# Kernel optimization log

Measured on AMD Instinct MI355X. Metric: run time of the kernel, lower is better.

## Reference

```python
import jax, jax.numpy as jnp
import numpy as np

EMB_W, COMMIT_W, ENT_W = 1.0, 0.25, 0.1  # loss weights from init_kwargs


def setup_inputs() -> dict:
    key = jax.random.key(0)
    k1, k2 = jax.random.split(key)
    B, H, W, D, K = 32, 32, 32, 64, 1024
    inputs = jax.random.normal(k1, (B, H, W, D), dtype=jnp.float32)
    # keras RandomUniform default: U(-0.05, 0.05)
    codebook = jax.random.uniform(k2, (K, D), dtype=jnp.float32, minval=-0.05, maxval=0.05)
    return {"inputs": inputs, "codebook": codebook}


def reference(inputs, codebook):
    # inputs: [B,H,W,D], codebook: [K,D]
    D = inputs.shape[-1]
    x = inputs.reshape(-1, D)  # [N,D]
    dist = (
        jnp.sum(x * x, axis=-1, keepdims=True)
        - 2.0 * (x @ codebook.T)
        + jnp.sum(codebook * codebook, axis=-1)
    )  # [N,K]
    tokens = jnp.argmin(dist, axis=-1)  # [N]
    emb = codebook[tokens].reshape(inputs.shape)  # [B,H,W,D]

    embedding_loss = EMB_W * jnp.mean((jax.lax.stop_gradient(emb) - inputs) ** 2)
    commitment_loss = COMMIT_W * jnp.mean((emb - jax.lax.stop_gradient(inputs)) ** 2)
    # 'entropy' loss as written in call(): mean over codebook of per-code min distance
    entropy_loss = ENT_W * jnp.mean(jnp.min(dist, axis=0))
    loss = embedding_loss + commitment_loss + entropy_loss

    # training=True path: straight-through estimator
    out = inputs + jax.lax.stop_gradient(emb - inputs)
    return out, loss
```

## Files before the change

### kernel.cpp

```cpp
#include <hip/hip_runtime.h>
#include <math.h>

#define NROWS 32768
#define NCODE 1024
#define AMB_CAP 8192
#define GAP_THRESH 1.5e-4f

typedef __attribute__((ext_vector_type(8))) short bf16x8;
typedef __attribute__((ext_vector_type(4))) float f32x4;

__device__ __forceinline__ unsigned short bf16_rne(float f) {
    unsigned u = __float_as_uint(f);
    unsigned r = u + 0x7FFFu + ((u >> 16) & 1u);
    return (unsigned short)(r >> 16);
}

typedef const __attribute__((address_space(1))) unsigned GU;
typedef __attribute__((address_space(3))) unsigned LU;
__device__ __forceinline__ void gl_lds16(const void* g, void* l) {
    __builtin_amdgcn_global_load_lds((GU*)g, (LU*)l, 16, 0, 0);
}
__device__ __forceinline__ void gl_lds4(const void* g, void* l) {
    __builtin_amdgcn_global_load_lds((GU*)g, (LU*)l, 4, 0, 0);
}

__global__ __launch_bounds__(256) void vq_prep(
    const float* __restrict__ cb, float* __restrict__ cn4,
    unsigned* __restrict__ minK, unsigned* __restrict__ counter,
    float* __restrict__ gsumsq, unsigned* __restrict__ ticket,
    unsigned short* __restrict__ wsB)
{
    int c = blockIdx.x * 256 + threadIdx.x;
    if (c == 0) { *counter = 0u; *gsumsq = 0.f; *ticket = 0u; }
    if (c >= NCODE) return;
    float v[64];
    const float4* src = (const float4*)(cb + (size_t)c * 64);
    float s = 0.f;
    #pragma unroll
    for (int i = 0; i < 16; i++) {
        float4 t = src[i];
        v[i*4+0] = t.x; v[i*4+1] = t.y; v[i*4+2] = t.z; v[i*4+3] = t.w;
        s += t.x*t.x + t.y*t.y + t.z*t.z + t.w*t.w;
    }
    cn4[c] = s + 4.0f;
    minK[c] = 0x7F800000u;
    int cc = c >> 6, ct = (c >> 4) & 3, cl = c & 15;
    #pragma unroll
    for (int q = 0; q < 4; q++) {
        int half = q & 1, lo = q >> 1;
        #pragma unroll
        for (int g = 0; g < 4; g++) {
            unsigned short u8[8] __attribute__((aligned(16)));
            #pragma unroll
            for (int j = 0; j < 8; j++) {
                float f = v[half*32 + g*8 + j];
                unsigned short h = bf16_rne(f);
                if (lo) h = bf16_rne(f - __uint_as_float((unsigned)h << 16));
                u8[j] = h;
            }
            size_t off = (size_t)cc * 8192 + ct * 2048 + q * 512 + (g * 16 + cl) * 8;
            *(uint4*)(wsB + off) = *(const uint4*)u8;
        }
    }
}

__global__ __launch_bounds__(256, 4) void vq_main(
    const float* __restrict__ x, const float* __restrict__ cb,
    const unsigned short* __restrict__ wsB, const float* __restrict__ cn4,
    float* __restrict__ out, unsigned* __restrict__ minK,
    unsigned* __restrict__ counter, int* __restrict__ amb,
    float* __restrict__ gsumsq)
{
    __shared__ __align__(16) unsigned char Bb[2][16384];
    __shared__ float cn4L[2][64];
    __shared__ unsigned scrE[1024];
    __shared__ int   tokS[64];
    __shared__ float redS[4];

    const int tid = threadIdx.x;
    const int lane = tid & 63;
    const int wi = tid >> 6;
    const int ln15 = lane & 15;
    const int q = lane >> 4;
    const int row0 = blockIdx.x * 64;
    const int rot = blockIdx.x & 15;

    #pragma unroll
    for (int jj = 0; jj < 4; jj++) scrE[jj*256 + tid] = 0x7F800000u;

    const char* wsBb = (const char*)wsB;
    {
        int wbase = (tid & ~63) * 16;
        #pragma unroll
        for (int i = 0; i < 4; i++)
            gl_lds16(wsBb + rot*16384 + (i*256 + tid)*16, (void*)&Bb[0][i*4096 + wbase]);
        if (wi == 0) gl_lds4(cn4 + rot*64 + lane, (void*)&cn4L[0][0]);
    }

    bf16x8 Ah0, Ah1, Al0, Al1;
    float xnm4[4];
    {
        const float* xr = x + (size_t)(row0 + wi*16 + ln15) * 64 + q * 8;
        float4 f0 = *(const float4*)xr;
        float4 f1 = *(const float4*)(xr + 4);
        float4 f2 = *(const float4*)(xr + 32);
        float4 f3 = *(const float4*)(xr + 36);
        float fa[8] = {f0.x,f0.y,f0.z,f0.w,f1.x,f1.y,f1.z,f1.w};
        float fb[8] = {f2.x,f2.y,f2.z,f2.w,f3.x,f3.y,f3.z,f3.w};
        unsigned short h[8]  __attribute__((aligned(16)));
        unsigned short l[8]  __attribute__((aligned(16)));
        unsigned short h2[8] __attribute__((aligned(16)));
        unsigned short l2[8] __attribute__((aligned(16)));
        float ss = 0.f;
        #pragma unroll
        for (int j = 0; j < 8; j++) {
            ss += fa[j]*fa[j] + fb[j]*fb[j];
            unsigned short hh = bf16_rne(fa[j]);
            h[j] = hh; l[j] = bf16_rne(fa[j] - __uint_as_float((unsigned)hh << 16));
            hh = bf16_rne(fb[j]);
            h2[j] = hh; l2[j] = bf16_rne(fb[j] - __uint_as_float((unsigned)hh << 16));
        }
        Ah0 = *(const bf16x8*)h;  Al0 = *(const bf16x8*)l;
        Ah1 = *(const bf16x8*)h2; Al1 = *(const bf16x8*)l2;
        ss += __shfl_xor(ss, 16);
        ss += __shfl_xor(ss, 32);
        #pragma unroll
        for (int r = 0; r < 4; r++)
            xnm4[r] = __shfl(ss, (q << 2) | r, 64) - 4.0f;
    }

    float d1[4], d2[4];
    int   i1[4];
    #pragma unroll
    for (int r = 0; r < 4; r++) { d1[r] = INFINITY; d2[r] = INFINITY; i1[r] = 0; }

    for (int s = 0; s < 16; s++) {
        __syncthreads();
        const int cb_ = s & 1, nb = (s + 1) & 1;
        const int cphys = (s + rot) & 15;
        if (s < 15) {
            const int cnx = (s + 1 + rot) & 15;
            int wbase = (tid & ~63) * 16;
            #pragma unroll
            for (int i = 0; i < 4; i++)
                gl_lds16(wsBb + cnx*16384 + (i*256 + tid)*16,
                         (void*)&Bb[nb][i*4096 + wbase]);
            if (wi == 0) gl_lds4(cn4 + cnx*64 + lane, (void*)&cn4L[nb][0]);
        }
        const unsigned char* buf = Bb[cb_];
        #pragma unroll
        for (int ct = 0; ct < 4; ct++) {
            bf16x8 Bh0 = *(const bf16x8*)(buf + ct*4096 +    0 + lane*16);
            bf16x8 Bh1 = *(const bf16x8*)(buf + ct*4096 + 1024 + lane*16);
            bf16x8 Bl0 = *(const bf16x8*)(buf + ct*4096 + 2048 + lane*16);
            bf16x8 Bl1 = *(const bf16x8*)(buf + ct*4096 + 3072 + lane*16);
            float cn4v = cn4L[cb_][ct*16 + ln15];
            int kid = cphys*64 + ct*16 + ln15;
            f32x4 acc = {0.f, 0.f, 0.f, 0.f};
            acc = __builtin_amdgcn_mfma_f32_16x16x32_bf16(Ah0, Bh0, acc, 0, 0, 0);
            acc = __builtin_amdgcn_mfma_f32_16x16x32_bf16(Ah1, Bh1, acc, 0, 0, 0);
            acc = __builtin_amdgcn_mfma_f32_16x16x32_bf16(Ah0, Bl0, acc, 0, 0, 0);
            acc = __builtin_amdgcn_mfma_f32_16x16x32_bf16(Ah1, Bl1, acc, 0, 0, 0);
            acc = __builtin_amdgcn_mfma_f32_16x16x32_bf16(Al0, Bh0, acc, 0, 0, 0);
            acc = __builtin_amdgcn_mfma_f32_16x16x32_bf16(Al1, Bh1, acc, 0, 0, 0);
            float cminv = INFINITY;
            #pragma unroll
            for (int r = 0; r < 4; r++) {
                float wv = fmaf(acc[r], -2.0f, cn4v);
                bool lt = wv < d1[r];
                d2[r] = lt ? d1[r] : fminf(d2[r], wv);
                i1[r] = lt ? kid   : i1[r];
                d1[r] = lt ? wv    : d1[r];
                cminv = fminf(cminv, wv + xnm4[r]);
            }
            cminv = fminf(cminv, __shfl_xor(cminv, 16));
            cminv = fminf(cminv, __shfl_xor(cminv, 32));
            if (q == ct) atomicMin(&scrE[kid], __float_as_uint(cminv));
        }
    }
    __syncthreads();

    #pragma unroll
    for (int d = 1; d < 16; d <<= 1) {
        #pragma unroll
        for (int r = 0; r < 4; r++) {
            float od1 = __shfl_xor(d1[r], d);
            int   oi1 = __shfl_xor(i1[r], d);
            float od2 = __shfl_xor(d2[r], d);
            bool take = (od1 < d1[r]) || (od1 == d1[r] && oi1 < i1[r]);
            float loser = take ? d1[r] : od1;
            d2[r] = fminf(fminf(d2[r], od2), loser);
            d1[r] = take ? od1 : d1[r];
            i1[r] = take ? oi1 : i1[r];
        }
    }
    if (ln15 == 0) {
        #pragma unroll
        for (int r = 0; r < 4; r++) {
            tokS[wi*16 + q*4 + r] = i1[r];
            if (d2[r] - d1[r] < GAP_THRESH) {
                unsigned idx = atomicAdd(counter, 1u);
                if (idx < AMB_CAP) {
                    amb[2*idx]   = row0 + wi*16 + q*4 + r;
                    amb[2*idx+1] = i1[r];
                }
            }
        }
    }
    __syncthreads();

    #pragma unroll
    for (int jj = 0; jj < 4; jj++) {
        int c = jj*256 + tid;
        unsigned u = scrE[c];
        if (u < minK[c]) atomicMin(&minK[c], u);
    }

    {
        int grow = tid >> 2, p = tid & 3;
        int tok = tokS[grow];
        const float4* cv = (const float4*)(cb + (size_t)tok*64 + p*16);
        const float4* xv = (const float4*)(x  + (size_t)(row0 + grow)*64 + p*16);
        float4* ov = (float4*)(out + (size_t)(row0 + grow)*64 + p*16);
        float acc2 = 0.f;
        #pragma unroll
        for (int i = 0; i < 4; i++) {
            float4 c = cv[i]; float4 xx = xv[i];
            ov[i] = c;
            float dx = c.x-xx.x, dy = c.y-xx.y, dz = c.z-xx.z, dw = c.w-xx.w;
            acc2 += dx*dx + dy*dy + dz*dz + dw*dw;
        }
        #pragma unroll
        for (int o = 32; o > 0; o >>= 1) acc2 += __shfl_down(acc2, o);
        if ((tid & 63) == 0) redS[tid >> 6] = acc2;
        __syncthreads();
        if (tid == 0) atomicAdd(gsumsq, redS[0] + redS[1] + redS[2] + redS[3]);
    }
}

__global__ __launch_bounds__(256) void vq_tail(
    const float* __restrict__ x, const float* __restrict__ cb,
    float* __restrict__ out, const unsigned* __restrict__ counter,
    const int* __restrict__ amb, float* __restrict__ gsumsq,
    unsigned* __restrict__ ticket, const unsigned* __restrict__ minK,
    float* __restrict__ out_loss)
{
    __shared__ double xs[64];
    __shared__ double bd[256];
    __shared__ int    bi[256];
    __shared__ unsigned lastS;
    __shared__ float redS[4];

    const int tid = threadIdx.x;

    unsigned cnt = *counter; if (cnt > AMB_CAP) cnt = AMB_CAP;
    for (unsigned i = blockIdx.x; i < cnt; i += gridDim.x) {
        int row = amb[2*i], oldk = amb[2*i+1];
        __syncthreads();
        if (tid < 64) xs[tid] = (double)x[(size_t)row*64 + tid];
        __syncthreads();
        double xn = 0.0;
        #pragma unroll 8
        for (int d = 0; d < 64; d++) xn += xs[d]*xs[d];
        double best = INFINITY; int bk = 1 << 30;
        #pragma unroll
        for (int j = 0; j < 4; j++) {
            int k = j*256 + tid;
            const float4* c4 = (const float4*)(cb + (size_t)k*64);
            double dot = 0.0, cn2 = 0.0;
            #pragma unroll
            for (int t = 0; t < 16; t++) {
                float4 cv = c4[t];
                double cx = (double)cv.x, cy = (double)cv.y, cz = (double)cv.z, cw = (double)cv.w;
                dot += xs[t*4+0]*cx + xs[t*4+1]*cy + xs[t*4+2]*cz + xs[t*4+3]*cw;
                cn2 += cx*cx + cy*cy + cz*cz + cw*cw;
            }
            double dist = (xn - 2.0*dot) + cn2;
            if (dist < best || (dist == best && k < bk)) { best = dist; bk = k; }
        }
        bd[tid] = best; bi[tid] = bk;
        __syncthreads();
        for (int s = 128; s > 0; s >>= 1) {
            if (tid < s) {
                double od = bd[tid+s]; int ok = bi[tid+s];
                if (od < bd[tid] || (od == bd[tid] && ok < bi[tid])) { bd[tid] = od; bi[tid] = ok; }
            }
            __syncthreads();
        }
        int bestk = bi[0];
        if (bestk != oldk) {
            double part = 0.0;
            if (tid < 64) {
                float cn = cb[(size_t)bestk*64 + tid];
                float co = cb[(size_t)oldk*64 + tid];
                out[(size_t)row*64 + tid] = cn;
                double dn = (double)cn - xs[tid];
                double dl = (double)co - xs[tid];
                part = dn*dn - dl*dl;
            }
            __syncthreads();
            bd[tid] = part;
            __syncthreads();
            for (int s = 128; s > 0; s >>= 1) {
                if (tid < s) bd[tid] += bd[tid+s];
                __syncthreads();
            }
            if (tid == 0) atomicAdd(gsumsq, (float)bd[0]);
        }
    }

    __syncthreads();
    if (tid == 0) {
        __threadfence();
        lastS = (atomicAdd(ticket, 1u) == (unsigned)(gridDim.x - 1)) ? 1u : 0u;
    }
    __syncthreads();
    if (lastS) {
        __threadfence();
        float s = 0.f;
        #pragma unroll
        for (int jj = 0; jj < 4; jj++)
            s += __uint_as_float(minK[jj*256 + tid]);
        #pragma unroll
        for (int o = 32; o > 0; o >>= 1) s += __shfl_down(s, o);
        if ((tid & 63) == 0) redS[tid >> 6] = s;
        __syncthreads();
        if (tid == 0) {
            float gs = atomicAdd(gsumsq, 0.0f);
            float tot = redS[0] + redS[1] + redS[2] + redS[3];
            out_loss[0] = 1.25f * (gs / 2097152.0f) + 0.1f * (tot / 1024.0f);
        }
    }
}

extern "C" void kernel_launch(void* const* d_in, const int* in_sizes, int n_in,
                              void* d_out, int out_size, void* d_ws, size_t ws_size,
                              hipStream_t stream) {
    const float* x  = (const float*)d_in[0];
    const float* cb = (const float*)d_in[1];
    float* out = (float*)d_out;

    char* ws = (char*)d_ws;
    unsigned*       counter = (unsigned*)ws;
    float*          gsumsq  = (float*)(ws + 4);
    unsigned*       ticket  = (unsigned*)(ws + 8);
    float*          cn4     = (float*)(ws + 1024);
    unsigned*       minK    = (unsigned*)(ws + 8192);
    int*            amb     = (int*)(ws + 16384);
    unsigned short* wsB     = (unsigned short*)(ws + 131072);

    vq_prep<<<4,   256, 0, stream>>>(cb, cn4, minK, counter, gsumsq, ticket, wsB);
    vq_main<<<512, 256, 0, stream>>>(x, cb, wsB, cn4, out, minK, counter, amb, gsumsq);
    vq_tail<<<64,  256, 0, stream>>>(x, cb, out, counter, amb, gsumsq, ticket, minK,
                                     out + 2097152);
}
```

Measured before the change: 136.2 us.

## Split codebook tiles across wave pairs with 512-thread blocks and merge argmins

Doubles the main kernel's block size to 8 waves. Each pair of waves now shares 16 input rows, and each wave of the pair processes half of every 64-code tile. The per-row top-2 results of the two halves are merged through shared memory before the ambiguity check and the gather. The prep kernel is relaunched as 16 blocks of 64 threads so more CUs share the codebook conversion. This is meant to raise wave-level parallelism and shorten the per-wave serial MFMA chain. The cost is duplicated A-operand conversion, an extra merge stage with a barrier, and possible occupancy limits from 512-thread blocks.

```diff
diff --git a/kernel.cpp b/kernel.cpp
--- a/kernel.cpp
+++ b/kernel.cpp
@@ -24,15 +24,14 @@
     __builtin_amdgcn_global_load_lds((GU*)g, (LU*)l, 4, 0, 0);
 }
 
-__global__ __launch_bounds__(256) void vq_prep(
+__global__ __launch_bounds__(64) void vq_prep(
     const float* __restrict__ cb, float* __restrict__ cn4,
     unsigned* __restrict__ minK, unsigned* __restrict__ counter,
     float* __restrict__ gsumsq, unsigned* __restrict__ ticket,
     unsigned short* __restrict__ wsB)
 {
-    int c = blockIdx.x * 256 + threadIdx.x;
+    int c = blockIdx.x * 64 + threadIdx.x;
     if (c == 0) { *counter = 0u; *gsumsq = 0.f; *ticket = 0u; }
-    if (c >= NCODE) return;
     float v[64];
     const float4* src = (const float4*)(cb + (size_t)c * 64);
     float s = 0.f;
@@ -64,7 +63,7 @@
     }
 }
 
-__global__ __launch_bounds__(256, 4) void vq_main(
+__global__ __launch_bounds__(512, 4) void vq_main(
     const float* __restrict__ x, const float* __restrict__ cb,
     const unsigned short* __restrict__ wsB, const float* __restrict__ cn4,
     float* __restrict__ out, unsigned* __restrict__ minK,
@@ -74,54 +73,57 @@
     __shared__ __align__(16) unsigned char Bb[2][16384];
     __shared__ float cn4L[2][64];
     __shared__ unsigned scrE[1024];
+    __shared__ float mD1[128], mD2[128];
+    __shared__ int   mI1[128];
     __shared__ int   tokS[64];
-    __shared__ float redS[4];
+    __shared__ float redS[8];
 
     const int tid = threadIdx.x;
     const int lane = tid & 63;
     const int wi = tid >> 6;
+    const int g = wi >> 1;
+    const int h = wi & 1;
     const int ln15 = lane & 15;
     const int q = lane >> 4;
     const int row0 = blockIdx.x * 64;
     const int rot = blockIdx.x & 15;
 
     #pragma unroll
-    for (int jj = 0; jj < 4; jj++) scrE[jj*256 + tid] = 0x7F800000u;
+    for (int jj = 0; jj < 2; jj++) scrE[jj*512 + tid] = 0x7F800000u;
 
     const char* wsBb = (const char*)wsB;
     {
         int wbase = (tid & ~63) * 16;
-        #pragma unroll
-        for (int i = 0; i < 4; i++)
-            gl_lds16(wsBb + rot*16384 + (i*256 + tid)*16, (void*)&Bb[0][i*4096 + wbase]);
+        gl_lds16(wsBb + rot*16384 +        tid*16, (void*)&Bb[0][wbase]);
+        gl_lds16(wsBb + rot*16384 + 8192 + tid*16, (void*)&Bb[0][8192 + wbase]);
         if (wi == 0) gl_lds4(cn4 + rot*64 + lane, (void*)&cn4L[0][0]);
     }
 
     bf16x8 Ah0, Ah1, Al0, Al1;
     float xnm4[4];
     {
-        const float* xr = x + (size_t)(row0 + wi*16 + ln15) * 64 + q * 8;
+        const float* xr = x + (size_t)(row0 + g*16 + ln15) * 64 + q * 8;
         float4 f0 = *(const float4*)xr;
         float4 f1 = *(const float4*)(xr + 4);
         float4 f2 = *(const float4*)(xr + 32);
         float4 f3 = *(const float4*)(xr + 36);
         float fa[8] = {f0.x,f0.y,f0.z,f0.w,f1.x,f1.y,f1.z,f1.w};
         float fb[8] = {f2.x,f2.y,f2.z,f2.w,f3.x,f3.y,f3.z,f3.w};
-        unsigned short h[8]  __attribute__((aligned(16)));
-        unsigned short l[8]  __attribute__((aligned(16)));
-        unsigned short h2[8] __attribute__((aligned(16)));
-        unsigned short l2[8] __attribute__((aligned(16)));
+        unsigned short hh8[8] __attribute__((aligned(16)));
+        unsigned short ll8[8] __attribute__((aligned(16)));
+        unsigned short h28[8] __attribute__((aligned(16)));
+        unsigned short l28[8] __attribute__((aligned(16)));
         float ss = 0.f;
         #pragma unroll
         for (int j = 0; j < 8; j++) {
             ss += fa[j]*fa[j] + fb[j]*fb[j];
             unsigned short hh = bf16_rne(fa[j]);
-            h[j] = hh; l[j] = bf16_rne(fa[j] - __uint_as_float((unsigned)hh << 16));
+            hh8[j] = hh; ll8[j] = bf16_rne(fa[j] - __uint_as_float((unsigned)hh << 16));
             hh = bf16_rne(fb[j]);
-            h2[j] = hh; l2[j] = bf16_rne(fb[j] - __uint_as_float((unsigned)hh << 16));
-        }
-        Ah0 = *(const bf16x8*)h;  Al0 = *(const bf16x8*)l;
-        Ah1 = *(const bf16x8*)h2; Al1 = *(const bf16x8*)l2;
+            h28[j] = hh; l28[j] = bf16_rne(fb[j] - __uint_as_float((unsigned)hh << 16));
+        }
+        Ah0 = *(const bf16x8*)hh8; Al0 = *(const bf16x8*)ll8;
+        Ah1 = *(const bf16x8*)h28; Al1 = *(const bf16x8*)l28;
         ss += __shfl_xor(ss, 16);
         ss += __shfl_xor(ss, 32);
         #pragma unroll
@@ -141,15 +143,14 @@
         if (s < 15) {
             const int cnx = (s + 1 + rot) & 15;
             int wbase = (tid & ~63) * 16;
-            #pragma unroll
-            for (int i = 0; i < 4; i++)
-                gl_lds16(wsBb + cnx*16384 + (i*256 + tid)*16,
-                         (void*)&Bb[nb][i*4096 + wbase]);
+            gl_lds16(wsBb + cnx*16384 +        tid*16, (void*)&Bb[nb][wbase]);
+            gl_lds16(wsBb + cnx*16384 + 8192 + tid*16, (void*)&Bb[nb][8192 + wbase]);
             if (wi == 0) gl_lds4(cn4 + cnx*64 + lane, (void*)&cn4L[nb][0]);
         }
         const unsigned char* buf = Bb[cb_];
         #pragma unroll
-        for (int ct = 0; ct < 4; ct++) {
+        for (int lct = 0; lct < 2; lct++) {
+            const int ct = 2*h + lct;
             bf16x8 Bh0 = *(const bf16x8*)(buf + ct*4096 +    0 + lane*16);
             bf16x8 Bh1 = *(const bf16x8*)(buf + ct*4096 + 1024 + lane*16);
             bf16x8 Bl0 = *(const bf16x8*)(buf + ct*4096 + 2048 + lane*16);
@@ -175,7 +176,7 @@
             }
             cminv = fminf(cminv, __shfl_xor(cminv, 16));
             cminv = fminf(cminv, __shfl_xor(cminv, 32));
-            if (q == ct) atomicMin(&scrE[kid], __float_as_uint(cminv));
+            if (q == lct) atomicMin(&scrE[kid], __float_as_uint(cminv));
         }
     }
     __syncthreads();
@@ -197,44 +198,58 @@
     if (ln15 == 0) {
         #pragma unroll
         for (int r = 0; r < 4; r++) {
-            tokS[wi*16 + q*4 + r] = i1[r];
-            if (d2[r] - d1[r] < GAP_THRESH) {
-                unsigned idx = atomicAdd(counter, 1u);
-                if (idx < AMB_CAP) {
-                    amb[2*idx]   = row0 + wi*16 + q*4 + r;
-                    amb[2*idx+1] = i1[r];
-                }
-            }
-        }
-    }
-    __syncthreads();
-
-    #pragma unroll
-    for (int jj = 0; jj < 4; jj++) {
-        int c = jj*256 + tid;
+            int idx = (g*16 + q*4 + r) * 2 + h;
+            mD1[idx] = d1[r]; mI1[idx] = i1[r]; mD2[idx] = d2[r];
+        }
+    }
+    __syncthreads();
+
+    if (tid < 64) {
+        float a1 = mD1[tid*2],   b1 = mD1[tid*2+1];
+        int   ai = mI1[tid*2],   bi = mI1[tid*2+1];
+        float a2 = mD2[tid*2],   b2 = mD2[tid*2+1];
+        bool ta = (a1 < b1) || (a1 == b1 && ai < bi);
+        float D1 = ta ? a1 : b1;
+        int   I1 = ta ? ai : bi;
+        float D2 = ta ? fminf(a2, b1) : fminf(b2, a1);
+        tokS[tid] = I1;
+        if (D2 - D1 < GAP_THRESH) {
+            unsigned idx = atomicAdd(counter, 1u);
+            if (idx < AMB_CAP) { amb[2*idx] = row0 + tid; amb[2*idx+1] = I1; }
+        }
+    }
+
+    #pragma unroll
+    for (int jj = 0; jj < 2; jj++) {
+        int c = jj*512 + tid;
         unsigned u = scrE[c];
         if (u < minK[c]) atomicMin(&minK[c], u);
     }
+    __syncthreads();
 
     {
-        int grow = tid >> 2, p = tid & 3;
-        int tok = tokS[grow];
-        const float4* cv = (const float4*)(cb + (size_t)tok*64 + p*16);
-        const float4* xv = (const float4*)(x  + (size_t)(row0 + grow)*64 + p*16);
-        float4* ov = (float4*)(out + (size_t)(row0 + grow)*64 + p*16);
         float acc2 = 0.f;
         #pragma unroll
-        for (int i = 0; i < 4; i++) {
-            float4 c = cv[i]; float4 xx = xv[i];
-            ov[i] = c;
+        for (int uu = 0; uu < 2; uu++) {
+            int u = uu*512 + tid;
+            int row = u >> 4, c4 = u & 15;
+            int tok = tokS[row];
+            float4 c = ((const float4*)(cb + (size_t)tok*64))[c4];
+            float4 xx = ((const float4*)(x + (size_t)(row0 + row)*64))[c4];
+            ((float4*)(out + (size_t)(row0 + row)*64))[c4] = c;
             float dx = c.x-xx.x, dy = c.y-xx.y, dz = c.z-xx.z, dw = c.w-xx.w;
             acc2 += dx*dx + dy*dy + dz*dz + dw*dw;
         }
         #pragma unroll
         for (int o = 32; o > 0; o >>= 1) acc2 += __shfl_down(acc2, o);
-        if ((tid & 63) == 0) redS[tid >> 6] = acc2;
-        __syncthreads();
-        if (tid == 0) atomicAdd(gsumsq, redS[0] + redS[1] + redS[2] + redS[3]);
+        if (lane == 0) redS[wi] = acc2;
+        __syncthreads();
+        if (tid == 0) {
+            float t = 0.f;
+            #pragma unroll
+            for (int w = 0; w < 8; w++) t += redS[w];
+            atomicAdd(gsumsq, t);
+        }
     }
 }
 
@@ -349,8 +364,8 @@
     int*            amb     = (int*)(ws + 16384);
     unsigned short* wsB     = (unsigned short*)(ws + 131072);
 
-    vq_prep<<<4,   256, 0, stream>>>(cb, cn4, minK, counter, gsumsq, ticket, wsB);
-    vq_main<<<512, 256, 0, stream>>>(x, cb, wsB, cn4, out, minK, counter, amb, gsumsq);
+    vq_prep<<<16,  64,  0, stream>>>(cb, cn4, minK, counter, gsumsq, ticket, wsB);
+    vq_main<<<512, 512, 0, stream>>>(x, cb, wsB, cn4, out, minK, counter, amb, gsumsq);
     vq_tail<<<64,  256, 0, stream>>>(x, cb, out, counter, amb, gsumsq, ticket, minK,
                                      out + 2097152);
 }
```

After: 130.6 us. -4.1%, faster.
